# Kernel tuning notes

Measured on AMD Instinct MI355X. Metric: run time of the kernel, lower is better.

Reference implementation:

```python
import jax, jax.numpy as jnp
import numpy as np

HIDDEN = 2048
HEADS = 16
HEAD_DIM = HIDDEN // HEADS  # 128
ROPE_BASE = 10000.0
RMS_EPS = 1e-6
MINUS_INF = -10000.0


def rms_norm(x, w):
    xf = x.astype(jnp.float32)
    var = jnp.mean(xf * xf, axis=-1, keepdims=True)
    return w * (x * jax.lax.rsqrt(var + RMS_EPS))


def rotate_half(x):
    x1, x2 = jnp.split(x, 2, axis=-1)
    return jnp.concatenate((-x2, x1), axis=-1)


def rope_tables(seq_len, dtype):
    inv_freq = 1.0 / (ROPE_BASE ** (jnp.arange(0, HEAD_DIM, 2, dtype=jnp.float32) / HEAD_DIM))
    t = jnp.arange(seq_len, dtype=jnp.float32)
    freqs = jnp.einsum('i,j->ij', t, inv_freq)           # [S, D/2]
    emb = jnp.concatenate((freqs, freqs), axis=-1)       # [S, D]
    return jnp.cos(emb).astype(dtype), jnp.sin(emb).astype(dtype)


def setup_inputs() -> dict:
    key = jax.random.key(0)
    ks = jax.random.split(key, 6)
    B, S, H = 2, 2048, HIDDEN
    x = jax.random.normal(ks[0], (B, S, H), dtype=jnp.float32) * 0.5
    norm_w = jnp.ones((H,), dtype=jnp.float32)
    scale = 0.02
    wq = jax.random.normal(ks[1], (H, H), dtype=jnp.float32) * scale
    wk = jax.random.normal(ks[2], (H, H), dtype=jnp.float32) * scale
    wv = jax.random.normal(ks[3], (H, H), dtype=jnp.float32) * scale
    wo = jax.random.normal(ks[4], (H, H), dtype=jnp.float32) * scale
    position_ids = jnp.broadcast_to(jnp.arange(S, dtype=jnp.int32), (B, S))
    return {"x": x, "norm_w": norm_w, "wq": wq, "wk": wk, "wv": wv,
            "wo": wo, "position_ids": position_ids}


def reference(x, norm_w, wq, wk, wv, wo, position_ids):
    B, S, H = x.shape
    h = rms_norm(x, norm_w)
    # torch Linear: y = h @ W.T, weight is [out, in]
    def proj(w):
        return jnp.einsum('bsd,od->bso', h, w).reshape(B, S, HEADS, HEAD_DIM).transpose(0, 2, 1, 3)
    q, k, v = proj(wq), proj(wk), proj(wv)  # [B, Hh, S, D]
    cos, sin = rope_tables(S, x.dtype)
    cos = cos[position_ids][:, None]  # [B, 1, S, D]
    sin = sin[position_ids][:, None]
    q = q * cos + rotate_half(q) * sin
    k = k * cos + rotate_half(k) * sin
    scores = jnp.einsum('bhqd,bhkd->bhqk', q, k) / jnp.sqrt(jnp.float32(HEAD_DIM))
    causal = jnp.tril(jnp.ones((S, S), dtype=bool))
    scores = scores + jnp.where(causal, 0.0, MINUS_INF).astype(scores.dtype)
    probs = jax.nn.softmax(scores, axis=-1)
    ctx = jnp.einsum('bhqk,bhkd->bhqd', probs, v)          # [B, Hh, S, D]
    ctx = ctx.transpose(0, 2, 1, 3).reshape(B, S, H)
    out = jnp.einsum('bsd,od->bso', ctx, wo)
    return out
```

## Files before the change

kernel.cpp:

```cpp
#include <hip/hip_runtime.h>
#include <hip/hip_bf16.h>
#include <stdint.h>

#define S_LEN   2048
#define BATCH   2
#define HID     2048
#define NHEADS  16
#define HDIM    128
#define ROWS    (BATCH * S_LEN)
#define QS      6144
#define ATT_SCALE 0.08838834764831843f

typedef __attribute__((ext_vector_type(8))) short s16x8;
typedef __attribute__((ext_vector_type(4))) float f32x4;

#define GLL16(gp, lp)                                                          \
  __builtin_amdgcn_global_load_lds(                                            \
      (__attribute__((address_space(1))) void*)(gp),                           \
      (__attribute__((address_space(3))) void*)(lp), 16, 0, 0)

__device__ __forceinline__ float bf2f(unsigned short u) {
  union { unsigned int i; float f; } v; v.i = ((unsigned int)u) << 16; return v.f;
}
__device__ __forceinline__ unsigned short f2bf(float f) {
  union { float f; unsigned int i; } v; v.f = f;
  unsigned int i = v.i;
  return (unsigned short)((i + 0x7FFFu + ((i >> 16) & 1u)) >> 16);
}
__device__ __forceinline__ void store_out(unsigned short* p, float v) { *p = f2bf(v); }
__device__ __forceinline__ void store_out(float* p, float v) { *p = v; }

__global__ __launch_bounds__(256) void cast4_kernel(const float* __restrict__ w0,
                                                    const float* __restrict__ w1,
                                                    const float* __restrict__ w2,
                                                    const float* __restrict__ w3,
                                                    unsigned short* __restrict__ dqkv,
                                                    unsigned short* __restrict__ dwo) {
  const int which = blockIdx.y;
  const float* src = (which == 0) ? w0 : (which == 1) ? w1 : (which == 2) ? w2 : w3;
  unsigned short* dst = (which < 3) ? dqkv + (size_t)which * HID * HID : dwo;
  int i = blockIdx.x * 256 + threadIdx.x;
  float4 v = ((const float4*)src)[i];
  ushort4 o;
  o.x = f2bf(v.x); o.y = f2bf(v.y); o.z = f2bf(v.z); o.w = f2bf(v.w);
  ((ushort4*)dst)[i] = o;
}

__global__ __launch_bounds__(256) void rmsnorm_kernel(const float* __restrict__ x,
                                                      const float* __restrict__ w,
                                                      unsigned short* __restrict__ h) {
  int row = blockIdx.x;
  int t = threadIdx.x;
  const float4* xr4 = (const float4*)(x + (size_t)row * HID);
  float4 a = xr4[t], b = xr4[t + 256];
  float ss = a.x*a.x + a.y*a.y + a.z*a.z + a.w*a.w
           + b.x*b.x + b.y*b.y + b.z*b.z + b.w*b.w;
#pragma unroll
  for (int off = 32; off >= 1; off >>= 1) ss += __shfl_xor(ss, off, 64);
  __shared__ float red[4];
  if ((t & 63) == 0) red[t >> 6] = ss;
  __syncthreads();
  float tot = red[0] + red[1] + red[2] + red[3];
  float rs = rsqrtf(tot * (1.0f / (float)HID) + 1e-6f);
  const float4* w4 = (const float4*)w;
  float4 wa = w4[t], wb = w4[t + 256];
  ushort4 oa, ob;
  oa.x = f2bf(a.x * wa.x * rs); oa.y = f2bf(a.y * wa.y * rs);
  oa.z = f2bf(a.z * wa.z * rs); oa.w = f2bf(a.w * wa.w * rs);
  ob.x = f2bf(b.x * wb.x * rs); ob.y = f2bf(b.y * wb.y * rs);
  ob.z = f2bf(b.z * wb.z * rs); ob.w = f2bf(b.w * wb.w * rs);
  ushort4* hr = (ushort4*)(h + (size_t)row * HID);
  hr[t] = oa; hr[t + 256] = ob;
}

__global__ void rope_tab_kernel(float* __restrict__ cost, float* __restrict__ sint) {
  int s = blockIdx.x, j = threadIdx.x;
  float inv = powf(10000.0f, -((float)j) / 64.0f);
  float ang = (float)s * inv;
  cost[s * 64 + j] = cosf(ang);
  sint[s * 64 + j] = sinf(ang);
}

__global__ __launch_bounds__(256) void rope_kernel(const int* __restrict__ pos_ids,
                                                   const float* __restrict__ cost,
                                                   const float* __restrict__ sint,
                                                   unsigned short* __restrict__ qkv) {
  int row = blockIdx.x;
  int p = pos_ids[row];
  int t = threadIdx.x;
  int head = t >> 4;
  int j0 = (t & 15) * 4;
  size_t base = (size_t)row * QS + head * HDIM;
  float4 c = *(const float4*)(cost + p * 64 + j0);
  float4 s = *(const float4*)(sint + p * 64 + j0);
#pragma unroll
  for (int which = 0; which < 2; which++) {
    unsigned short* ptr = qkv + base + which * HID;
    float sc = which ? 1.0f : ATT_SCALE;
    ushort4 v1 = *(ushort4*)(ptr + j0);
    ushort4 v2 = *(ushort4*)(ptr + 64 + j0);
    ushort4 o1, o2;
    o1.x = f2bf((bf2f(v1.x) * c.x - bf2f(v2.x) * s.x) * sc);
    o1.y = f2bf((bf2f(v1.y) * c.y - bf2f(v2.y) * s.y) * sc);
    o1.z = f2bf((bf2f(v1.z) * c.z - bf2f(v2.z) * s.z) * sc);
    o1.w = f2bf((bf2f(v1.w) * c.w - bf2f(v2.w) * s.w) * sc);
    o2.x = f2bf((bf2f(v2.x) * c.x + bf2f(v1.x) * s.x) * sc);
    o2.y = f2bf((bf2f(v2.y) * c.y + bf2f(v1.y) * s.y) * sc);
    o2.z = f2bf((bf2f(v2.z) * c.z + bf2f(v1.z) * s.z) * sc);
    o2.w = f2bf((bf2f(v2.w) * c.w + bf2f(v1.w) * s.w) * sc);
    *(ushort4*)(ptr + j0) = o1;
    *(ushort4*)(ptr + 64 + j0) = o2;
  }
}

__global__ __launch_bounds__(256) void transpose_v_kernel(const unsigned short* __restrict__ qkv,
                                                          unsigned short* __restrict__ vt) {
  __shared__ unsigned short tile[64][72];
  const int stile = blockIdx.x, dt = blockIdx.y, bh = blockIdx.z;
  const int t = threadIdx.x;
  const int b = bh >> 4, h = bh & 15;
  const int s0 = stile * 64;
  const unsigned short* src = qkv + (size_t)(b * S_LEN + s0) * QS + 2 * HID + h * HDIM + dt * 64;
#pragma unroll
  for (int it = 0; it < 2; it++) {
    int sl = (t >> 3) + 32 * it;
    int dl = (t & 7) * 8;
    *(s16x8*)&tile[sl][dl] = *(const s16x8*)(src + (size_t)sl * QS + dl);
  }
  __syncthreads();
#pragma unroll
  for (int it = 0; it < 2; it++) {
    int dl = (t >> 3) + 32 * it;
    int sl8 = (t & 7) * 8;
    s16x8 o;
#pragma unroll
    for (int jj = 0; jj < 8; jj++) o[jj] = (short)tile[sl8 + jj][dl];
    *(s16x8*)(vt + (size_t)(bh * 128 + dt * 64 + dl) * S_LEN + s0 + sl8) = o;
  }
}

#define SH(kt, bi, kk2) {                                                      \
    const unsigned short* sa_ = aQ + (size_t)(kt) * 64 + (kk2) * 32;           \
    const unsigned short* sb_ = bQ + (size_t)(kt) * 64 + (kk2) * 32;           \
    char* da_ = qsm + ((bi) * 2 + (kk2)) * 32768 + tid * 16;                   \
    GLL16(sa_, da_);                                                           \
    GLL16(sa_ + (size_t)128 * K, da_ + 8192);                                  \
    GLL16(sb_, da_ + 16384);                                                   \
    GLL16(sb_ + (size_t)128 * K, da_ + 16384 + 8192);                          \
  }

__global__ __launch_bounds__(512, 2) void gemm_qk_kernel(const unsigned short* __restrict__ A,
                                                         const unsigned short* __restrict__ B,
                                                         unsigned short* __restrict__ C,
                                                         int K, int N) {
  __shared__ __align__(16) unsigned short Qsm[2][2][2][256 * 32];
  const int bm = blockIdx.y, bn = blockIdx.x;
  const int tid = threadIdx.x;
  const int w = tid >> 6, wr = w >> 2, wc = w & 3;
  const int l = tid & 63, g = l >> 4, r = l & 15;
  const int KT = K >> 6;

  const int srow = tid >> 2;
  const int sg = (tid & 3) ^ ((tid >> 2) & 3) ^ ((tid >> 4) & 3);
  const unsigned short* aQ = A + (size_t)(bm * 256 + srow) * K + sg * 8;
  const unsigned short* bQ = B + (size_t)(bn * 256 + srow) * K + sg * 8;
  char* const qsm = (char*)Qsm;

  f32x4 zero = {0.f, 0.f, 0.f, 0.f};
  f32x4 acc[8][4];
#pragma unroll
  for (int mi = 0; mi < 8; mi++)
#pragma unroll
    for (int ni = 0; ni < 4; ni++) acc[mi][ni] = zero;

  const int ro = ((g ^ (r & 3) ^ ((r >> 2) & 3)) << 4);
  const int aOff = (wr * 128 + r) * 64 + ro;
  const int bOff = 16384 + (wc * 64 + r) * 64 + ro;

  SH(0, 0, 0); SH(0, 0, 1);

  for (int kt = 0; kt < KT; ++kt) {
    const int buf = kt & 1;
    const bool more = (kt + 1 < KT);
    const char* l0 = qsm + (buf * 2 + 0) * 32768;
    const char* l1 = qsm + (buf * 2 + 1) * 32768;

    asm volatile("s_waitcnt vmcnt(4)" ::: "memory");
    __builtin_amdgcn_s_barrier();
    __builtin_amdgcn_sched_barrier(0);
    s16x8 a[4], b[4];
#pragma unroll
    for (int ni = 0; ni < 4; ni++) b[ni] = *(const s16x8*)(l0 + bOff + ni * 1024);
#pragma unroll
    for (int i = 0; i < 4; i++) a[i] = *(const s16x8*)(l0 + aOff + i * 1024);
    if (more) SH(kt + 1, buf ^ 1, 0);
    __builtin_amdgcn_s_setprio(1);
#pragma unroll
    for (int ni = 0; ni < 4; ni++)
#pragma unroll
      for (int i = 0; i < 4; i++)
        acc[i][ni] = __builtin_amdgcn_mfma_f32_16x16x32_bf16(a[i], b[ni], acc[i][ni], 0, 0, 0);
    __builtin_amdgcn_s_setprio(0);

    s16x8 a2[4];
#pragma unroll
    for (int i = 0; i < 4; i++) a2[i] = *(const s16x8*)(l0 + aOff + (4 + i) * 1024);
    __builtin_amdgcn_s_setprio(1);
#pragma unroll
    for (int ni = 0; ni < 4; ni++)
#pragma unroll
      for (int i = 0; i < 4; i++)
        acc[4 + i][ni] = __builtin_amdgcn_mfma_f32_16x16x32_bf16(a2[i], b[ni], acc[4 + i][ni], 0, 0, 0);
    __builtin_amdgcn_s_setprio(0);

    if (more) { asm volatile("s_waitcnt vmcnt(4)" ::: "memory"); }
    else      { asm volatile("s_waitcnt vmcnt(0)" ::: "memory"); }
    __builtin_amdgcn_s_barrier();
    __builtin_amdgcn_sched_barrier(0);
#pragma unroll
    for (int ni = 0; ni < 4; ni++) b[ni] = *(const s16x8*)(l1 + bOff + ni * 1024);
#pragma unroll
    for (int i = 0; i < 4; i++) a[i] = *(const s16x8*)(l1 + aOff + i * 1024);
    if (more) SH(kt + 1, buf ^ 1, 1);
    __builtin_amdgcn_s_setprio(1);
#pragma unroll
    for (int ni = 0; ni < 4; ni++)
#pragma unroll
      for (int i = 0; i < 4; i++)
        acc[i][ni] = __builtin_amdgcn_mfma_f32_16x16x32_bf16(a[i], b[ni], acc[i][ni], 0, 0, 0);
    __builtin_amdgcn_s_setprio(0);

#pragma unroll
    for (int i = 0; i < 4; i++) a2[i] = *(const s16x8*)(l1 + aOff + (4 + i) * 1024);
    __builtin_amdgcn_s_setprio(1);
#pragma unroll
    for (int ni = 0; ni < 4; ni++)
#pragma unroll
      for (int i = 0; i < 4; i++)
        acc[4 + i][ni] = __builtin_amdgcn_mfma_f32_16x16x32_bf16(a2[i], b[ni], acc[4 + i][ni], 0, 0, 0);
    __builtin_amdgcn_s_setprio(0);
  }

#pragma unroll
  for (int mi = 0; mi < 8; mi++)
#pragma unroll
    for (int ni = 0; ni < 4; ni++) {
      const int crow = bm * 256 + wr * 128 + mi * 16 + g * 4;
      const int ccol = bn * 256 + wc * 64 + ni * 16 + r;
#pragma unroll
      for (int j = 0; j < 4; j++)
        store_out(&C[(size_t)(crow + j) * N + ccol], acc[mi][ni][j]);
    }
}
#undef SH

#define SA(kt, bi) {                                                           \
    const unsigned short* s_ = aS + (size_t)(kt) * 64;                         \
    char* d_ = (char*)Ab[bi] + tid * 16;                                       \
    GLL16(s_, d_);                                                             \
    GLL16(s_ + (size_t)64 * K, d_ + 8192);                                     \
  }
#define SB(kt, bi, hf) {                                                       \
    const unsigned short* s_ = bS + (size_t)(hf) * 128 * K + (size_t)(kt) * 64;\
    char* d_ = (char*)Bb[bi] + (hf) * 16384 + tid * 16;                        \
    GLL16(s_, d_);                                                             \
    GLL16(s_ + (size_t)64 * K, d_ + 8192);                                     \
  }

template <typename OutT, int NI>
__global__ __launch_bounds__(512, 1) void gemm8_kernel(const unsigned short* __restrict__ A,
                                                       const unsigned short* __restrict__ B,
                                                       OutT* __restrict__ C, int K, int N) {
  __shared__ __align__(16) unsigned short Ab[3][128 * 64];
  __shared__ __align__(16) unsigned short Bb[3][NI * 64 * 64];
  const int bm = blockIdx.y, bn = blockIdx.x;
  const int tid = threadIdx.x;
  const int w = tid >> 6, wr = w >> 2, wc = w & 3;
  const int l = tid & 63, g = l >> 4, r = l & 15;
  const int KT = K >> 6;

  const int srow = tid >> 3;
  const int sgr = (tid & 7) ^ (srow & 7);
  const unsigned short* aS = A + (size_t)(bm * 128 + srow) * K + sgr * 8;
  const unsigned short* bS = B + (size_t)(bn * (NI * 64) + srow) * K + sgr * 8;

  f32x4 zero = {0.f, 0.f, 0.f, 0.f};
  f32x4 acc[4][NI];
#pragma unroll
  for (int mi = 0; mi < 4; mi++)
#pragma unroll
    for (int ni = 0; ni < NI; ni++) acc[mi][ni] = zero;

  const int swx = (r & 7) << 4;
  const int ks0 = (g << 4) ^ swx;
  const int ks1 = ((4 | g) << 4) ^ swx;
  const int aOff = (wr * 64 + r) * 128;
  const int bOff = (wc * (NI * 16) + r) * 128;

  SA(0, 0); SB(0, 0, 0); if (NI == 4) SB(0, 0, 1);
  SA(1, 1); SB(1, 1, 0); if (NI == 4) SB(1, 1, 1);

  int cur = 0;
  for (int kt = 0; kt < KT; ++kt) {
    const int b2 = (cur >= 1) ? cur - 1 : cur + 2;
    if (kt == KT - 1)      { asm volatile("s_waitcnt vmcnt(0)" ::: "memory"); }
    else if (NI == 4)      { asm volatile("s_waitcnt vmcnt(6)" ::: "memory"); }
    else                   { asm volatile("s_waitcnt vmcnt(4)" ::: "memory"); }
    __builtin_amdgcn_s_barrier();
    __builtin_amdgcn_sched_barrier(0);
    const char* lA = (const char*)Ab[cur];
    const char* lB = (const char*)Bb[cur];
    const bool more = (kt + 2 < KT);

    s16x8 a[4][2], b[NI][2];
#pragma unroll
    for (int mi = 0; mi < 4; mi++) {
      a[mi][0] = *(const s16x8*)(lA + aOff + mi * 2048 + ks0);
      a[mi][1] = *(const s16x8*)(lA + aOff + mi * 2048 + ks1);
    }
#pragma unroll
    for (int ni = 0; ni < NI / 2; ni++) {
      b[ni][0] = *(const s16x8*)(lB + bOff + ni * 2048 + ks0);
      b[ni][1] = *(const s16x8*)(lB + bOff + ni * 2048 + ks1);
    }
    if (more) { SA(kt + 2, b2); if (NI == 4) SB(kt + 2, b2, 0); }
    __builtin_amdgcn_s_setprio(1);
#pragma unroll
    for (int kk = 0; kk < 2; kk++)
#pragma unroll
      for (int ni = 0; ni < NI / 2; ni++)
#pragma unroll
        for (int mi = 0; mi < 4; mi++)
          acc[mi][ni] = __builtin_amdgcn_mfma_f32_16x16x32_bf16(a[mi][kk], b[ni][kk], acc[mi][ni], 0, 0, 0);
    __builtin_amdgcn_s_setprio(0);
    __builtin_amdgcn_sched_barrier(0);

#pragma unroll
    for (int ni = NI / 2; ni < NI; ni++) {
      b[ni][0] = *(const s16x8*)(lB + bOff + ni * 2048 + ks0);
      b[ni][1] = *(const s16x8*)(lB + bOff + ni * 2048 + ks1);
    }
    if (more) { if (NI == 4) { SB(kt + 2, b2, 1); } else { SB(kt + 2, b2, 0); } }
    __builtin_amdgcn_s_setprio(1);
#pragma unroll
    for (int kk = 0; kk < 2; kk++)
#pragma unroll
      for (int ni = NI / 2; ni < NI; ni++)
#pragma unroll
        for (int mi = 0; mi < 4; mi++)
          acc[mi][ni] = __builtin_amdgcn_mfma_f32_16x16x32_bf16(a[mi][kk], b[ni][kk], acc[mi][ni], 0, 0, 0);
    __builtin_amdgcn_s_setprio(0);
    cur = (cur == 2) ? 0 : cur + 1;
  }

#pragma unroll
  for (int mi = 0; mi < 4; mi++)
#pragma unroll
    for (int ni = 0; ni < NI; ni++) {
      const int crow = bm * 128 + wr * 64 + mi * 16 + g * 4;
      const int ccol = bn * (NI * 64) + wc * (NI * 16) + ni * 16 + r;
#pragma unroll
      for (int j = 0; j < 4; j++)
        store_out(&C[(size_t)(crow + j) * N + ccol], acc[mi][ni][j]);
    }
}

__global__ __launch_bounds__(256, 4) void attn_kernel(const unsigned short* __restrict__ QKV,
                                                      const unsigned short* __restrict__ VT,
                                                      unsigned short* __restrict__ O) {
  __shared__ __align__(16) unsigned short Ksm[64 * 128];
  __shared__ __align__(16) unsigned short VTsm[128 * 64];
  __shared__ __align__(16) unsigned short Psm[4 * 16 * 64];
  const int bid = blockIdx.x;
  const int grp = bid & 7, idx = bid >> 3;
  const int qt = 31 - (idx >> 2);
  const int bh = (grp << 2) | (idx & 3);
  const int b = bh >> 4, hd = bh & 15;
  const int tid = threadIdx.x, w = tid >> 6, l = tid & 63, g = l >> 4, r = l & 15;
  const int qbs = qt * 64 + w * 16;

  const unsigned short* qp = QKV + (size_t)(b * S_LEN + qbs + r) * QS + hd * HDIM;
  s16x8 qf[4];
#pragma unroll
  for (int ks = 0; ks < 4; ks++) qf[ks] = *(const s16x8*)(qp + ks * 32 + g * 8);

  float mreg[4], lreg[4];
  f32x4 zero = {0.f, 0.f, 0.f, 0.f};
  f32x4 oacc[8];
#pragma unroll
  for (int jj = 0; jj < 4; jj++) { mreg[jj] = -1e30f; lreg[jj] = 0.f; }
#pragma unroll
  for (int di = 0; di < 8; di++) oacc[di] = zero;

  const int cK = tid & 15, rowK = tid >> 4;
  const unsigned short* kp_base = QKV + (size_t)(b * S_LEN + rowK) * QS + HID + hd * HDIM
                                  + ((cK ^ (rowK & 7)) << 3);
  const int cV = tid & 7, dV = tid >> 3;
  const unsigned short* vp_base = VT + (size_t)(bh * 128 + dV) * S_LEN + ((cV ^ (dV & 7)) << 3);
  char* const ksm_c = (char*)Ksm;
  char* const vtsm_c = (char*)VTsm;
  char* const psm_w = (char*)Psm + w * 2048;

#define STAGE(kt)                                                              \
  {                                                                            \
    const unsigned short* kp_ = kp_base + (size_t)((kt) * 64) * QS;            \
    const unsigned short* vp_ = vp_base + (kt) * 64;                           \
    GLL16(kp_,                      ksm_c + tid * 16);                         \
    GLL16(kp_ + (size_t)16 * QS,    ksm_c + (tid + 256) * 16);                 \
    GLL16(kp_ + (size_t)32 * QS,    ksm_c + (tid + 512) * 16);                 \
    GLL16(kp_ + (size_t)48 * QS,    ksm_c + (tid + 768) * 16);                 \
    GLL16(vp_,                      vtsm_c + tid * 16);                        \
    GLL16(vp_ + (size_t)32 * S_LEN, vtsm_c + (tid + 256) * 16);                \
    GLL16(vp_ + (size_t)64 * S_LEN, vtsm_c + (tid + 512) * 16);                \
    GLL16(vp_ + (size_t)96 * S_LEN, vtsm_c + (tid + 768) * 16);                \
  }

  const int nt = qt + 1;
  STAGE(0);

  for (int kt2 = 0; kt2 < nt; kt2++) {
    asm volatile("s_waitcnt vmcnt(0)" ::: "memory");
    __builtin_amdgcn_s_barrier();
    __builtin_amdgcn_sched_barrier(0);

    f32x4 sacc[4];
#pragma unroll
    for (int ni = 0; ni < 4; ni++) sacc[ni] = zero;
#pragma unroll
    for (int ni = 0; ni < 4; ni++) {
      const int krow = ni * 16 + r;
      const int swz = (krow & 7) << 4;
      const char* kb2 = ksm_c + krow * 256;
#pragma unroll
      for (int ks = 0; ks < 4; ks++) {
        s16x8 kf = *(const s16x8*)(kb2 + ((ks * 64 + g * 16) ^ swz));
        sacc[ni] = __builtin_amdgcn_mfma_f32_16x16x32_bf16(qf[ks], kf, sacc[ni], 0, 0, 0);
      }
    }

    const bool domask = (kt2 == qt);
    float mrow[4];
#pragma unroll
    for (int jj = 0; jj < 4; jj++) mrow[jj] = -1e30f;
#pragma unroll
    for (int ni = 0; ni < 4; ni++)
#pragma unroll
      for (int jj = 0; jj < 4; jj++) {
        float sval = sacc[ni][jj];
        if (domask && (kt2 * 64 + ni * 16 + r) > (qbs + g * 4 + jj)) sval = -1e30f;
        sacc[ni][jj] = sval;
        mrow[jj] = fmaxf(mrow[jj], sval);
      }
#pragma unroll
    for (int jj = 0; jj < 4; jj++) {
#pragma unroll
      for (int off = 8; off >= 1; off >>= 1)
        mrow[jj] = fmaxf(mrow[jj], __shfl_xor(mrow[jj], off, 64));
    }
    float corr[4];
#pragma unroll
    for (int jj = 0; jj < 4; jj++) {
      float mn = fmaxf(mreg[jj], mrow[jj]);
      corr[jj] = __expf(mreg[jj] - mn);
      mreg[jj] = mn;
      float sm = 0.f;
#pragma unroll
      for (int ni = 0; ni < 4; ni++) {
        float p2 = __expf(sacc[ni][jj] - mn);
        sacc[ni][jj] = p2;
        sm += p2;
      }
#pragma unroll
      for (int off = 8; off >= 1; off >>= 1) sm += __shfl_xor(sm, off, 64);
      lreg[jj] = lreg[jj] * corr[jj] + sm;
    }
#pragma unroll
    for (int di = 0; di < 8; di++)
#pragma unroll
      for (int jj = 0; jj < 4; jj++) oacc[di][jj] *= corr[jj];

#pragma unroll
    for (int ni = 0; ni < 4; ni++)
#pragma unroll
      for (int jj = 0; jj < 4; jj++) {
        int prow = g * 4 + jj;
        int byte = (prow * 128 + ((ni * 16 + r) << 1)) ^ ((prow & 7) << 4);
        *(unsigned short*)(psm_w + byte) = f2bf(sacc[ni][jj]);
      }

#pragma unroll
    for (int ksl = 0; ksl < 2; ksl++) {
      s16x8 pa = *(const s16x8*)(psm_w + ((r * 128 + ((ksl * 32 + g * 8) << 1)) ^ ((r & 7) << 4)));
      const int kgran = ksl * 4 + g;
#pragma unroll
      for (int di = 0; di < 8; di++) {
        const int d = di * 16 + r;
        s16x8 vf = *(const s16x8*)(vtsm_c + d * 128 + ((kgran ^ (d & 7)) << 4));
        oacc[di] = __builtin_amdgcn_mfma_f32_16x16x32_bf16(pa, vf, oacc[di], 0, 0, 0);
      }
    }

    __builtin_amdgcn_s_barrier();
    if (kt2 + 1 < nt) STAGE(kt2 + 1);
  }
#undef STAGE

#pragma unroll
  for (int di = 0; di < 8; di++)
#pragma unroll
    for (int jj = 0; jj < 4; jj++) {
      int orow = qbs + g * 4 + jj;
      O[(size_t)(b * S_LEN + orow) * HID + hd * HDIM + di * 16 + r] =
          f2bf(oacc[di][jj] / lreg[jj]);
    }
}

extern "C" void kernel_launch(void* const* d_in, const int* in_sizes, int n_in,
                              void* d_out, int out_size, void* d_ws, size_t ws_size,
                              hipStream_t stream) {
  const float* x      = (const float*)d_in[0];
  const float* norm_w = (const float*)d_in[1];
  const float* wq     = (const float*)d_in[2];
  const float* wk     = (const float*)d_in[3];
  const float* wv     = (const float*)d_in[4];
  const float* wo     = (const float*)d_in[5];
  const int*   pos    = (const int*)d_in[6];
  float* out = (float*)d_out;

  char* ws = (char*)d_ws;
  const size_t WQKV_B = (size_t)3 * HID * HID * 2;
  const size_t WO_B   = (size_t)HID * HID * 2;
  const size_t H_B    = (size_t)ROWS * HID * 2;
  const size_t QKV_B  = (size_t)ROWS * QS * 2;

  unsigned short* wqkvb = (unsigned short*)(ws);
  unsigned short* vt    = (unsigned short*)(ws);
  unsigned short* wob   = (unsigned short*)(ws + WQKV_B);
  unsigned short* h     = (unsigned short*)(ws + WQKV_B + WO_B);
  unsigned short* qkv   = (unsigned short*)(ws + WQKV_B + WO_B + H_B);
  float* cost = (float*)(ws + WQKV_B + WO_B + H_B + QKV_B);
  float* sint = cost + (size_t)S_LEN * 64;

  dim3 cgrid(HID * HID / 4 / 256, 4);
  cast4_kernel<<<cgrid, 256, 0, stream>>>(wq, wk, wv, wo, wqkvb, wob);
  rope_tab_kernel<<<S_LEN, 64, 0, stream>>>(cost, sint);
  rmsnorm_kernel<<<ROWS, 256, 0, stream>>>(x, norm_w, h);

  dim3 qkgrid(2 * HID / 256, ROWS / 256);
  gemm_qk_kernel<<<qkgrid, 512, 0, stream>>>(h, wqkvb, qkv, HID, QS);

  dim3 vgrid(HID / 256, ROWS / 128);
  gemm8_kernel<unsigned short, 4><<<vgrid, 512, 0, stream>>>(
      h, wqkvb + (size_t)2 * HID * HID, qkv + 2 * HID, HID, QS);

  dim3 tgrid(S_LEN / 64, 2, BATCH * NHEADS);
  transpose_v_kernel<<<tgrid, 256, 0, stream>>>(qkv, vt);

  rope_kernel<<<ROWS, 256, 0, stream>>>(pos, cost, sint, qkv);

  attn_kernel<<<1024, 256, 0, stream>>>(qkv, vt, h );

  dim3 ogrid(HID / 128, ROWS / 128);
  gemm8_kernel<float, 2><<<ogrid, 512, 0, stream>>>(h, wob, out, HID, HID);
}
```

Measured before the change: 295.1 us.

## Double-buffer attention K/V tiles, use exp2 softmax with lazy rescale, widen out-proj tile

The attention kernel now double-buffers its K and V^T shared-memory tiles, so the next tile is prefetched right after the barrier and the second barrier per iteration is dropped. Softmax switches to exp2, with log2(e) folded into the Q scale in the RoPE kernel, and only rescales the running max and accumulators when a row max grows by more than a threshold. P is converted with packed bf16 conversions. The output projection uses a wider N tile (NI=4). Shared memory per block doubles and launch bounds drop to 2 blocks per CU, which may reduce occupancy.

```diff
diff --git a/kernel.cpp b/kernel.cpp
--- a/kernel.cpp
+++ b/kernel.cpp
@@ -10,6 +10,7 @@
 #define ROWS    (BATCH * S_LEN)
 #define QS      6144
 #define ATT_SCALE 0.08838834764831843f
+#define LOG2E     1.4426950408889634f
 
 typedef __attribute__((ext_vector_type(8))) short s16x8;
 typedef __attribute__((ext_vector_type(4))) float f32x4;
@@ -96,7 +97,7 @@
 #pragma unroll
   for (int which = 0; which < 2; which++) {
     unsigned short* ptr = qkv + base + which * HID;
-    float sc = which ? 1.0f : ATT_SCALE;
+    float sc = which ? 1.0f : (ATT_SCALE * LOG2E);
     ushort4 v1 = *(ushort4*)(ptr + j0);
     ushort4 v2 = *(ushort4*)(ptr + 64 + j0);
     ushort4 o1, o2;
@@ -365,11 +366,11 @@
     }
 }
 
-__global__ __launch_bounds__(256, 4) void attn_kernel(const unsigned short* __restrict__ QKV,
+__global__ __launch_bounds__(256, 2) void attn_kernel(const unsigned short* __restrict__ QKV,
                                                       const unsigned short* __restrict__ VT,
                                                       unsigned short* __restrict__ O) {
-  __shared__ __align__(16) unsigned short Ksm[64 * 128];
-  __shared__ __align__(16) unsigned short VTsm[128 * 64];
+  __shared__ __align__(16) unsigned short Ksm[2][64 * 128];
+  __shared__ __align__(16) unsigned short VTsm[2][128 * 64];
   __shared__ __align__(16) unsigned short Psm[4 * 16 * 64];
   const int bid = blockIdx.x;
   const int grp = bid & 7, idx = bid >> 3;
@@ -397,31 +398,38 @@
                                   + ((cK ^ (rowK & 7)) << 3);
   const int cV = tid & 7, dV = tid >> 3;
   const unsigned short* vp_base = VT + (size_t)(bh * 128 + dV) * S_LEN + ((cV ^ (dV & 7)) << 3);
-  char* const ksm_c = (char*)Ksm;
-  char* const vtsm_c = (char*)VTsm;
+  char* const ksm0 = (char*)Ksm;
+  char* const vtsm0 = (char*)VTsm;
   char* const psm_w = (char*)Psm + w * 2048;
 
-#define STAGE(kt)                                                              \
+#define STAGE(kt, bufi)                                                        \
   {                                                                            \
     const unsigned short* kp_ = kp_base + (size_t)((kt) * 64) * QS;            \
     const unsigned short* vp_ = vp_base + (kt) * 64;                           \
-    GLL16(kp_,                      ksm_c + tid * 16);                         \
-    GLL16(kp_ + (size_t)16 * QS,    ksm_c + (tid + 256) * 16);                 \
-    GLL16(kp_ + (size_t)32 * QS,    ksm_c + (tid + 512) * 16);                 \
-    GLL16(kp_ + (size_t)48 * QS,    ksm_c + (tid + 768) * 16);                 \
-    GLL16(vp_,                      vtsm_c + tid * 16);                        \
-    GLL16(vp_ + (size_t)32 * S_LEN, vtsm_c + (tid + 256) * 16);                \
-    GLL16(vp_ + (size_t)64 * S_LEN, vtsm_c + (tid + 512) * 16);                \
-    GLL16(vp_ + (size_t)96 * S_LEN, vtsm_c + (tid + 768) * 16);                \
+    char* kd_ = ksm0 + (bufi) * 16384;                                         \
+    char* vd_ = vtsm0 + (bufi) * 16384;                                        \
+    GLL16(kp_,                      kd_ + tid * 16);                           \
+    GLL16(kp_ + (size_t)16 * QS,    kd_ + (tid + 256) * 16);                   \
+    GLL16(kp_ + (size_t)32 * QS,    kd_ + (tid + 512) * 16);                   \
+    GLL16(kp_ + (size_t)48 * QS,    kd_ + (tid + 768) * 16);                   \
+    GLL16(vp_,                      vd_ + tid * 16);                           \
+    GLL16(vp_ + (size_t)32 * S_LEN, vd_ + (tid + 256) * 16);                   \
+    GLL16(vp_ + (size_t)64 * S_LEN, vd_ + (tid + 512) * 16);                   \
+    GLL16(vp_ + (size_t)96 * S_LEN, vd_ + (tid + 768) * 16);                   \
   }
 
   const int nt = qt + 1;
-  STAGE(0);
+  STAGE(0, 0);
 
   for (int kt2 = 0; kt2 < nt; kt2++) {
+    const int buf = kt2 & 1;
     asm volatile("s_waitcnt vmcnt(0)" ::: "memory");
     __builtin_amdgcn_s_barrier();
     __builtin_amdgcn_sched_barrier(0);
+    if (kt2 + 1 < nt) STAGE(kt2 + 1, buf ^ 1);
+
+    const char* ksm_c = ksm0 + buf * 16384;
+    const char* vtsm_c = vtsm0 + buf * 16384;
 
     f32x4 sacc[4];
 #pragma unroll
@@ -438,55 +446,64 @@
       }
     }
 
-    const bool domask = (kt2 == qt);
+    if (kt2 == qt) {
+#pragma unroll
+      for (int ni = 0; ni < 4; ni++)
+#pragma unroll
+        for (int jj = 0; jj < 4; jj++)
+          if ((kt2 * 64 + ni * 16 + r) > (qbs + g * 4 + jj)) sacc[ni][jj] = -1e30f;
+    }
+
     float mrow[4];
 #pragma unroll
-    for (int jj = 0; jj < 4; jj++) mrow[jj] = -1e30f;
-#pragma unroll
-    for (int ni = 0; ni < 4; ni++)
-#pragma unroll
-      for (int jj = 0; jj < 4; jj++) {
-        float sval = sacc[ni][jj];
-        if (domask && (kt2 * 64 + ni * 16 + r) > (qbs + g * 4 + jj)) sval = -1e30f;
-        sacc[ni][jj] = sval;
-        mrow[jj] = fmaxf(mrow[jj], sval);
-      }
+    for (int jj = 0; jj < 4; jj++)
+      mrow[jj] = fmaxf(fmaxf(sacc[0][jj], sacc[1][jj]), fmaxf(sacc[2][jj], sacc[3][jj]));
 #pragma unroll
     for (int jj = 0; jj < 4; jj++) {
 #pragma unroll
       for (int off = 8; off >= 1; off >>= 1)
         mrow[jj] = fmaxf(mrow[jj], __shfl_xor(mrow[jj], off, 64));
     }
-    float corr[4];
+    bool grow = false;
+#pragma unroll
+    for (int jj = 0; jj < 4; jj++) grow = grow || (mrow[jj] > mreg[jj] + 8.0f);
+    if (__any(grow)) {
+#pragma unroll
+      for (int jj = 0; jj < 4; jj++) {
+        float mn = fmaxf(mreg[jj], mrow[jj]);
+        float corr = exp2f(mreg[jj] - mn);
+        mreg[jj] = mn;
+        lreg[jj] *= corr;
+#pragma unroll
+        for (int di = 0; di < 8; di++) oacc[di][jj] *= corr;
+      }
+    }
 #pragma unroll
     for (int jj = 0; jj < 4; jj++) {
-      float mn = fmaxf(mreg[jj], mrow[jj]);
-      corr[jj] = __expf(mreg[jj] - mn);
-      mreg[jj] = mn;
       float sm = 0.f;
 #pragma unroll
       for (int ni = 0; ni < 4; ni++) {
-        float p2 = __expf(sacc[ni][jj] - mn);
+        float p2 = exp2f(sacc[ni][jj] - mreg[jj]);
         sacc[ni][jj] = p2;
         sm += p2;
       }
 #pragma unroll
       for (int off = 8; off >= 1; off >>= 1) sm += __shfl_xor(sm, off, 64);
-      lreg[jj] = lreg[jj] * corr[jj] + sm;
-    }
-#pragma unroll
-    for (int di = 0; di < 8; di++)
-#pragma unroll
-      for (int jj = 0; jj < 4; jj++) oacc[di][jj] *= corr[jj];
-
-#pragma unroll
-    for (int ni = 0; ni < 4; ni++)
-#pragma unroll
-      for (int jj = 0; jj < 4; jj++) {
-        int prow = g * 4 + jj;
-        int byte = (prow * 128 + ((ni * 16 + r) << 1)) ^ ((prow & 7) << 4);
-        *(unsigned short*)(psm_w + byte) = f2bf(sacc[ni][jj]);
-      }
+      lreg[jj] += sm;
+    }
+
+#pragma unroll
+    for (int ni = 0; ni < 4; ni++) {
+      unsigned int pk01, pk23;
+      asm("v_cvt_pk_bf16_f32 %0, %1, %2" : "=v"(pk01) : "v"(sacc[ni][0]), "v"(sacc[ni][1]));
+      asm("v_cvt_pk_bf16_f32 %0, %1, %2" : "=v"(pk23) : "v"(sacc[ni][2]), "v"(sacc[ni][3]));
+      const int col2 = (ni * 16 + r) << 1;
+      const int pr0 = g * 4;
+      *(unsigned short*)(psm_w + (((pr0 + 0) * 128 + col2) ^ (((pr0 + 0) & 7) << 4))) = (unsigned short)pk01;
+      *(unsigned short*)(psm_w + (((pr0 + 1) * 128 + col2) ^ (((pr0 + 1) & 7) << 4))) = (unsigned short)(pk01 >> 16);
+      *(unsigned short*)(psm_w + (((pr0 + 2) * 128 + col2) ^ (((pr0 + 2) & 7) << 4))) = (unsigned short)pk23;
+      *(unsigned short*)(psm_w + (((pr0 + 3) * 128 + col2) ^ (((pr0 + 3) & 7) << 4))) = (unsigned short)(pk23 >> 16);
+    }
 
 #pragma unroll
     for (int ksl = 0; ksl < 2; ksl++) {
@@ -499,9 +516,6 @@
         oacc[di] = __builtin_amdgcn_mfma_f32_16x16x32_bf16(pa, vf, oacc[di], 0, 0, 0);
       }
     }
-
-    __builtin_amdgcn_s_barrier();
-    if (kt2 + 1 < nt) STAGE(kt2 + 1);
   }
 #undef STAGE
 
@@ -560,6 +574,6 @@
 
   attn_kernel<<<1024, 256, 0, stream>>>(qkv, vt, h );
 
-  dim3 ogrid(HID / 128, ROWS / 128);
-  gemm8_kernel<float, 2><<<ogrid, 512, 0, stream>>>(h, wob, out, HID, HID);
-}
+  dim3 ogrid(HID / 256, ROWS / 128);
+  gemm8_kernel<float, 4><<<ogrid, 512, 0, stream>>>(h, wob, out, HID, HID);
+}
```

New measurement: 284.6 us. 3.6% less time.
